# Kernel tuning notes

Hardware: AMD Instinct MI355X
Metric: run time of the kernel (lower is better)

## Reference

```python
import jax, jax.numpy as jnp
import numpy as np
import math

B, L, DM = 2, 2048, 1536
H, FD = 12, 16          # num_heads, feature_dim
DV = DM // H            # head_dim = 128
D2 = FD * FD            # expanded Taylor feature dim = 256
CHUNK = 128
EPS = 1e-12
LN_EPS = 1e-5


def setup_inputs() -> dict:
    key = jax.random.key(0)
    ks = jax.random.split(key, 5)
    s = lambda fan_in: 1.0 / math.sqrt(fan_in)
    return {
        "hidden_states": jax.random.normal(ks[0], (B, L, DM), jnp.float32),
        "Wq": jax.random.normal(ks[1], (DM, H * FD), jnp.float32) * s(DM),
        "Wk": jax.random.normal(ks[2], (DM, H * FD), jnp.float32) * s(DM),
        "Wv": jax.random.normal(ks[3], (DM, H * DV), jnp.float32) * s(DM),
        "Wo": jax.random.normal(ks[4], (H * DV, DM), jnp.float32) * s(H * DV),
        "ln_q_g": jnp.ones((H * FD,), jnp.float32),
        "ln_q_b": jnp.zeros((H * FD,), jnp.float32),
        "ln_k_g": jnp.ones((H * FD,), jnp.float32),
        "ln_k_b": jnp.zeros((H * FD,), jnp.float32),
    }


def _layernorm(x, g, b):
    mu = x.mean(-1, keepdims=True)
    var = ((x - mu) ** 2).mean(-1, keepdims=True)
    return (x - mu) * jax.lax.rsqrt(var + LN_EPS) * g + b


def _taylor_exp(x):
    # x: (b, h, l, d) -> flattened outer product / sqrt(d): (b, h, l, d*d)
    x2 = x[..., :, None] * x[..., None, :]
    return x2.reshape(*x.shape[:-1], -1) / math.sqrt(FD)


def _rebased_forward(hidden_states, Wq, Wk, Wv, Wo, ln_q_g, ln_q_b, ln_k_g, ln_k_b):
    b, l, _ = hidden_states.shape
    q = _layernorm(hidden_states @ Wq, ln_q_g, ln_q_b)
    k = _layernorm(hidden_states @ Wk, ln_k_g, ln_k_b)
    v = hidden_states @ Wv
    # (b, l, h*d) -> (b, h, l, d)
    q = q.reshape(b, l, H, FD).transpose(0, 2, 1, 3)
    k = k.reshape(b, l, H, FD).transpose(0, 2, 1, 3)
    v = v.reshape(b, l, H, DV).transpose(0, 2, 1, 3)
    q2 = _taylor_exp(q)  # (b, h, l, D2)
    k2 = _taylor_exp(k)

    nC = l // CHUNK
    # chunk-major layout for scan: (nC, b, h, C, .)
    q2c = q2.reshape(b, H, nC, CHUNK, D2).transpose(2, 0, 1, 3, 4)
    k2c = k2.reshape(b, H, nC, CHUNK, D2).transpose(2, 0, 1, 3, 4)
    vc = v.reshape(b, H, nC, CHUNK, DV).transpose(2, 0, 1, 3, 4)
    mask = jnp.tril(jnp.ones((CHUNK, CHUNK), q2.dtype))  # causal within chunk

    S0 = jnp.zeros((b, H, D2, DV), q2.dtype)  # running sum of k2^T v
    z0 = jnp.zeros((b, H, D2), q2.dtype)      # running sum of k2

    def step(carry, inp):
        S, z = carry
        qc, kc, vcur = inp
        A = jnp.einsum("bhcd,bhed->bhce", qc, kc) * mask  # intra-chunk scores
        num = jnp.einsum("bhcd,bhdv->bhcv", qc, S) + jnp.einsum("bhce,bhev->bhcv", A, vcur)
        den = jnp.einsum("bhcd,bhd->bhc", qc, z) + A.sum(-1)
        o = num / (den[..., None] + EPS)
        S = S + jnp.einsum("bhed,bhev->bhdv", kc, vcur)
        z = z + kc.sum(2)
        return (S, z), o

    _, o = jax.lax.scan(step, (S0, z0), (q2c, k2c, vc))
    # (nC, b, h, C, dv) -> (b, l, h*dv)
    o = o.transpose(1, 2, 0, 3, 4).reshape(b, H, l, DV).transpose(0, 2, 1, 3).reshape(b, l, H * DV)
    return o @ Wo


def reference(hidden_states, Wq, Wk, Wv, Wo, ln_q_g, ln_q_b, ln_k_g, ln_k_b):
    return _rebased_forward(hidden_states, Wq, Wk, Wv, Wo, ln_q_g, ln_q_b, ln_k_g, ln_k_b)
```

## Files before the change

### kernel.cpp

```cpp
#include <hip/hip_runtime.h>
#include <hip/hip_bf16.h>
#include <math.h>

#define Bc   2
#define Lc   2048
#define DMc  1536
#define Hc   12
#define FDc  16
#define DVc  128
#define D2c  256
#define CHK  128
#define NCH  16
#define ROWS (Bc*Lc)
#define HFD  (Hc*FDc)
#define HDV  (Hc*DVc)
#define NQK  (2*HFD)
#define NPRJ (NQK + HDV)

typedef __bf16 bf16x8 __attribute__((ext_vector_type(8)));
typedef float f32x4 __attribute__((ext_vector_type(4)));

__device__ __forceinline__ float bf2f(unsigned short u) {
    return __uint_as_float(((unsigned int)u) << 16);
}
__device__ __forceinline__ unsigned short f2bf(float v) {
    unsigned int u = __float_as_uint(v);
    unsigned int r = (u + 0x7FFFu + ((u >> 16) & 1u)) >> 16;
    return (unsigned short)r;
}
__device__ __forceinline__ unsigned int pack2(unsigned short a, unsigned short b) {
    return (unsigned int)a | ((unsigned int)b << 16);
}
__device__ __forceinline__ float ldin(const void* p, size_t i, int isf32) {
    return isf32 ? ((const float*)p)[i] : bf2f(((const unsigned short*)p)[i]);
}

#define GLL16(g, l) __builtin_amdgcn_global_load_lds( \
    (const __attribute__((address_space(1))) unsigned int*)(g), \
    (__attribute__((address_space(3))) unsigned int*)(l), 16, 0, 0)

__global__ void probe_dtype(const unsigned short* __restrict__ hs, int* __restrict__ flag) {
    const int tid = threadIdx.x;
    int sane = 0;
    for (int i = tid; i < 1024; i += 256) {
        unsigned short b = hs[2 * i];
        int e = (b >> 7) & 0xFF;
        if (e >= 97 && e <= 157) sane++;
    }
    __shared__ int tot;
    if (tid == 0) tot = 0;
    __syncthreads();
    atomicAdd(&tot, sane);
    __syncthreads();
    if (tid == 0) *flag = (tot >= 614) ? 0 : 1;
}

__global__ __launch_bounds__(256) void conv_bf16(const void* __restrict__ X,
                                                 unsigned short* __restrict__ Y,
                                                 int n4, const int* __restrict__ flagp) {
    const int f = *flagp;
    int i = blockIdx.x * 256 + threadIdx.x;
    if (i >= n4) return;
    if (f) {
        float4 x = ((const float4*)X)[i];
        ushort4 y;
        y.x = f2bf(x.x); y.y = f2bf(x.y); y.z = f2bf(x.z); y.w = f2bf(x.w);
        ((ushort4*)Y)[i] = y;
    } else {
        ((ushort4*)Y)[i] = ((const ushort4*)X)[i];
    }
}

__global__ __launch_bounds__(256) void convT_all(const void* __restrict__ Wq,
                                                 const void* __restrict__ Wk,
                                                 const void* __restrict__ Wv,
                                                 const void* __restrict__ Wo,
                                                 unsigned short* __restrict__ Wqkvt,
                                                 unsigned short* __restrict__ Wot,
                                                 const int* __restrict__ flagp) {
    const int f = *flagp;
    __shared__ float tile[64][65];
    const int t = threadIdx.x;
    int id = blockIdx.x;
    const void* W; unsigned short* Wt; int rows, cols, bx, by;
    if (id < 72)       { W = Wq; Wt = Wqkvt;                          rows = DMc; cols = HFD; bx = (id % 3) * 64;  by = (id / 3) * 64; }
    else if (id < 144) { id -= 72;  W = Wk; Wt = Wqkvt + (size_t)HFD * DMc; rows = DMc; cols = HFD; bx = (id % 3) * 64;  by = (id / 3) * 64; }
    else if (id < 720) { id -= 144; W = Wv; Wt = Wqkvt + (size_t)NQK * DMc; rows = DMc; cols = HDV; bx = (id % 24) * 64; by = (id / 24) * 64; }
    else               { id -= 720; W = Wo; Wt = Wot;                 rows = HDV; cols = DMc; bx = (id % 24) * 64; by = (id / 24) * 64; }
#pragma unroll
    for (int u = 0; u < 16; u++) {
        int idx = t + u * 256;
        int r = idx >> 6, c = idx & 63;
        tile[r][c] = ldin(W, (size_t)(by + r) * cols + bx + c, f);
    }
    __syncthreads();
#pragma unroll
    for (int u = 0; u < 16; u++) {
        int idx = t + u * 256;
        int r = idx >> 6, c = idx & 63;
        Wt[(size_t)(bx + r) * rows + by + c] = f2bf(tile[c][r]);
    }
}

__global__ __launch_bounds__(512) void gemm_mfma_bt(const unsigned short* __restrict__ A,
                                                    const unsigned short* __restrict__ Bt,
                                                    void* __restrict__ C,
                                                    int M, int N, int K,
                                                    int ldc,
                                                    int cMode, const int* __restrict__ flagp,
                                                    unsigned short* __restrict__ vTout) {
    const int f = *flagp;
    __shared__ __align__(16) unsigned char smem[32768];
    unsigned short* As = (unsigned short*)smem;
    unsigned short* Bsu = As + 8192;
    f32x4* scr4 = (f32x4*)smem;

    const int tid = threadIdx.x;
    const int wave = tid >> 6, lane = tid & 63;
    const int kgrp = wave >> 2;
    const int w4 = wave & 3;
    const int lin = blockIdx.y * gridDim.x + blockIdx.x;
    const int nwg = gridDim.x * gridDim.y;
    const int swz = (lin & 7) * (nwg >> 3) + (lin >> 3);
    const int row0 = (swz / gridDim.x) * 128, col0 = (swz % gridDim.x) * 128;
    const int wrow = (w4 >> 1) * 64, wcol = (w4 & 1) * 64;
    const int mlane = lane & 15, quad = lane >> 4;
    const int kHalf = K >> 1;

    const unsigned short* Ab = A + (size_t)row0 * K + (size_t)kgrp * kHalf;
    const unsigned short* Bb = Bt + (size_t)col0 * K + (size_t)kgrp * kHalf;
    const int t256 = tid & 255;
    const int r0 = t256 >> 2;
    const int kc = (t256 & 3) * 8;
    const size_t off0 = (size_t)r0 * K + kc;
    const size_t off1 = (size_t)(r0 + 64) * K + kc;
    char* AsW = (char*)As + kgrp * 8192 + w4 * 1024;
    char* BsW = (char*)Bsu + kgrp * 8192 + w4 * 1024;
    const int ldsBase = kgrp * 4096;

    f32x4 acc[4][4] = {};

    for (int k0 = 0; k0 < kHalf; k0 += 32) {
        GLL16(Ab + off0 + k0, AsW);
        GLL16(Ab + off1 + k0, AsW + 4096);
        GLL16(Bb + off0 + k0, BsW);
        GLL16(Bb + off1 + k0, BsW + 4096);
        __syncthreads();
        bf16x8 a[4], b[4];
#pragma unroll
        for (int i = 0; i < 4; i++)
            a[i] = *(const bf16x8*)&As[ldsBase + (wrow + i * 16 + mlane) * 32 + quad * 8];
#pragma unroll
        for (int j = 0; j < 4; j++)
            b[j] = *(const bf16x8*)&Bsu[ldsBase + (wcol + j * 16 + mlane) * 32 + quad * 8];
#pragma unroll
        for (int i = 0; i < 4; i++)
#pragma unroll
            for (int j = 0; j < 4; j++)
                acc[i][j] = __builtin_amdgcn_mfma_f32_16x16x32_bf16(a[i], b[j], acc[i][j], 0, 0, 0);
        __syncthreads();
    }

    {
        const int col = (wave & 1) * 64 + lane;
        if (kgrp == 1 && w4 < 2) {
#pragma unroll
            for (int i = 0; i < 4; i++)
#pragma unroll
                for (int j = 0; j < 4; j++)
                    scr4[(i * 4 + j) * 128 + col] = acc[i][j];
        }
        __syncthreads();
        if (kgrp == 0 && w4 < 2) {
#pragma unroll
            for (int i = 0; i < 4; i++)
#pragma unroll
                for (int j = 0; j < 4; j++)
                    acc[i][j] += scr4[(i * 4 + j) * 128 + col];
        }
        __syncthreads();
        if (kgrp == 1 && w4 >= 2) {
#pragma unroll
            for (int i = 0; i < 4; i++)
#pragma unroll
                for (int j = 0; j < 4; j++)
                    scr4[(i * 4 + j) * 128 + col] = acc[i][j];
        }
        __syncthreads();
        if (kgrp == 0 && w4 >= 2) {
#pragma unroll
            for (int i = 0; i < 4; i++)
#pragma unroll
                for (int j = 0; j < 4; j++)
                    acc[i][j] += scr4[(i * 4 + j) * 128 + col];
        }
    }
    if (kgrp != 0) return;

    float* Cf = nullptr;
    unsigned short* Cb16 = nullptr;
    bool doT = false;
    int tOff = 0;
    if (cMode == 0) Cf = (float*)C;
    else if (cMode == 1) Cb16 = (unsigned short*)C;
    else if (cMode == 2) { if (f) Cf = (float*)C; else Cb16 = (unsigned short*)C; }
    else if (cMode == 4) {
        if (col0 < NQK) Cf = (float*)C;
        else { doT = true; tOff = NQK; }
    }
    if (cMode <= 3 && vTout) doT = true;

#pragma unroll
    for (int i = 0; i < 4; i++)
#pragma unroll
        for (int j = 0; j < 4; j++) {
            const int col = col0 + wcol + j * 16 + mlane;
            if (Cf) {
#pragma unroll
                for (int r = 0; r < 4; r++) {
                    const int row = row0 + wrow + i * 16 + quad * 4 + r;
                    Cf[(size_t)row * ldc + col] = acc[i][j][r];
                }
            } else if (Cb16) {
#pragma unroll
                for (int r = 0; r < 4; r++) {
                    const int row = row0 + wrow + i * 16 + quad * 4 + r;
                    Cb16[(size_t)row * ldc + col] = f2bf(acc[i][j][r]);
                }
            }
            if (doT) {
                ushort4 pk;
                pk.x = f2bf(acc[i][j][0]); pk.y = f2bf(acc[i][j][1]);
                pk.z = f2bf(acc[i][j][2]); pk.w = f2bf(acc[i][j][3]);
                *(ushort4*)(vTout + (size_t)(col - tOff) * M + row0 + wrow + i * 16 + quad * 4) = pk;
            }
        }
}

__global__ __launch_bounds__(192) void ln_kernel(const float* __restrict__ qk,
                                                 float* __restrict__ q, float* __restrict__ k,
                                                 const void* __restrict__ gq,
                                                 const void* __restrict__ bq,
                                                 const void* __restrict__ gk,
                                                 const void* __restrict__ bk,
                                                 const int* __restrict__ flagp) {
    const int f = *flagp;
    const int row = blockIdx.x, t = threadIdx.x;
    float vq = qk[(size_t)row * NQK + t];
    float vk = qk[(size_t)row * NQK + HFD + t];
    float s[4] = {vq, vq * vq, vk, vk * vk};
    __shared__ float part[4][3];
    const int w = t >> 6, lane = t & 63;
#pragma unroll
    for (int i = 0; i < 4; i++) {
        float v = s[i];
        for (int off = 32; off; off >>= 1) v += __shfl_down(v, off);
        if (lane == 0) part[i][w] = v;
    }
    __syncthreads();
    float sq  = part[0][0] + part[0][1] + part[0][2];
    float sq2 = part[1][0] + part[1][1] + part[1][2];
    float sk  = part[2][0] + part[2][1] + part[2][2];
    float sk2 = part[3][0] + part[3][1] + part[3][2];
    const float inv = 1.0f / (float)HFD;
    float muq = sq * inv, muk = sk * inv;
    float varq = sq2 * inv - muq * muq;
    float vark = sk2 * inv - muk * muk;
    float oq = (vq - muq) * rsqrtf(varq + 1e-5f) * ldin(gq, t, f) + ldin(bq, t, f);
    float ok = (vk - muk) * rsqrtf(vark + 1e-5f) * ldin(gk, t, f) + ldin(bk, t, f);
    q[(size_t)row * HFD + t] = oq;
    k[(size_t)row * HFD + t] = ok;
}

__global__ __launch_bounds__(256) void state_prefix_mfma(const float* __restrict__ kn,
                                                         const unsigned short* __restrict__ vT,
                                                         unsigned short* __restrict__ St,
                                                         float* __restrict__ zc) {
    const int bx = blockIdx.x;
    const int by = blockIdx.y;
    const int bh = blockIdx.z;
    const int h = bh % Hc, b = bh / Hc;
    const int t0 = bx * 16;
    const int tid = threadIdx.x;
    const int wave = tid >> 6, lane = tid & 63;
    const int mlane = lane & 15, quad = lane >> 4;

    __shared__ __align__(16) float kcs[CHK * FDc];
    __shared__ __align__(16) unsigned short K2t[16 * 136];
    __shared__ __align__(16) unsigned short Vs[64 * 136];
    __shared__ float zp[16][17];
    __shared__ float zpre[16];
    if (tid < 16) zpre[tid] = 0.f;

    f32x4 acc = {};
    const int kr = tid >> 1, khf = tid & 1;
    const int d2l = tid & 15, cg = tid >> 4;
    const int vrow = tid >> 2, vseg = tid & 3;
    const int dvL = wave * 16 + mlane;

    for (int n = 0; n < NCH; n++) {
        const int row0 = b * Lc + n * CHK;
        __syncthreads();
        {
            const float4* src = (const float4*)(kn + (size_t)(row0 + kr) * HFD + h * FDc + khf * 8);
            *(float4*)(kcs + kr * 16 + khf * 8)     = src[0];
            *(float4*)(kcs + kr * 16 + khf * 8 + 4) = src[1];
            const uint4* g = (const uint4*)(vT + (size_t)(h * 128 + by * 64 + vrow) * ROWS + row0 + vseg * 32);
            *(uint4*)(Vs + vrow * 136 + vseg * 32)      = g[0];
            *(uint4*)(Vs + vrow * 136 + vseg * 32 + 8)  = g[1];
            *(uint4*)(Vs + vrow * 136 + vseg * 32 + 16) = g[2];
            *(uint4*)(Vs + vrow * 136 + vseg * 32 + 24) = g[3];
        }
        __syncthreads();
        {
            float zs_ = 0.f;
            unsigned short pk[8];
#pragma unroll
            for (int u = 0; u < 8; u++) {
                int c = cg * 8 + u;
                float p = kcs[c * 16 + bx] * kcs[c * 16 + d2l] * 0.25f;
                zs_ += p;
                pk[u] = f2bf(p);
            }
            uint4 w;
            w.x = pack2(pk[0], pk[1]); w.y = pack2(pk[2], pk[3]);
            w.z = pack2(pk[4], pk[5]); w.w = pack2(pk[6], pk[7]);
            *(uint4*)(K2t + d2l * 136 + cg * 8) = w;
            zp[d2l][cg] = zs_;
        }
        __syncthreads();
        {
            size_t base = (((size_t)(bh * NCH + n) * 16 + bx) * 128) * 16;
            int dv = by * 64 + dvL;
            ushort4 pk;
            pk.x = f2bf(acc[0]); pk.y = f2bf(acc[1]);
            pk.z = f2bf(acc[2]); pk.w = f2bf(acc[3]);
            *(ushort4*)(St + base + (size_t)dv * 16 + quad * 4) = pk;
            if (tid < 16) {
                float s = 0.f;
#pragma unroll
                for (int c = 0; c < 16; c++) s += zp[tid][c];
                if (by == 0)
                    zc[(size_t)(bh * NCH + n) * D2c + t0 + tid] = zpre[tid];
                zpre[tid] += s;
            }
        }
        {
#pragma unroll
            for (int ks = 0; ks < 4; ks++) {
                bf16x8 a = *(const bf16x8*)(K2t + mlane * 136 + ks * 32 + quad * 8);
                bf16x8 bfr = *(const bf16x8*)(Vs + dvL * 136 + ks * 32 + quad * 8);
                acc = __builtin_amdgcn_mfma_f32_16x16x32_bf16(a, bfr, acc, 0, 0, 0);
            }
        }
    }
}

__global__ __launch_bounds__(256) void chunk_out_mfma(const float* __restrict__ qn,
                                                      const float* __restrict__ kn,
                                                      const unsigned short* __restrict__ St,
                                                      const float* __restrict__ z,
                                                      const unsigned short* __restrict__ vT,
                                                      unsigned short* __restrict__ o) {
    const int blk = blockIdx.x;
    const int n = blk & 15, bh = blk >> 4;
    const int h = bh % Hc, b = bh / Hc;
    const int row0 = b * Lc + n * CHK;
    const int tid = threadIdx.x;
    const int wave = tid >> 6, lane = tid & 63;
    const int mlane = lane & 15, quad = lane >> 4;
    const int wrow = (wave >> 1) * 64, wcol = (wave & 1) * 64;

    __shared__ __align__(16) unsigned char lds[61952];
    float* Qs   = (float*)lds;
    float* zs   = (float*)(lds + 8192);
    float* denp = (float*)(lds + 9216);
    float* dinv = (float*)(lds + 10240);
    unsigned char* U = lds + 10752;
    unsigned short* Q2s = (unsigned short*)U;
    unsigned short* Sts = (unsigned short*)(U + 10240);
    unsigned short* Kb  = (unsigned short*)U;
    unsigned short* Qb  = (unsigned short*)(U + 8192);
    unsigned short* At  = (unsigned short*)(U + 16384);
    unsigned short* Vs  = (unsigned short*)U;

    {
        int r = tid >> 1, hf = tid & 1;
        const float4* src = (const float4*)(qn + (size_t)(row0 + r) * HFD + h * FDc + hf * 8);
        *(float4*)(Qs + r * 16 + hf * 8)     = src[0];
        *(float4*)(Qs + r * 16 + hf * 8 + 4) = src[1];
        if (tid < 64)
            ((float4*)zs)[tid] = ((const float4*)(z + ((size_t)bh * NCH + n) * D2c))[tid];
    }
    __syncthreads();

    const int qc = tid >> 1, qhalf = tid & 1;
    float qr[16];
#pragma unroll
    for (int ff = 0; ff < 16; ff++) qr[ff] = Qs[qc * 16 + ff];

    f32x4 acc[4][4] = {};
    float den1 = 0.f;
    const unsigned short* Stb = St + ((size_t)bh * NCH + n) * ((size_t)D2c * DVc);

    for (int k0 = 0; k0 < 256; k0 += 32) {
        {
            unsigned short pk[16];
#pragma unroll
            for (int kk = 0; kk < 16; kk++) {
                int d2 = k0 + qhalf * 16 + kk;
                float val = qr[d2 >> 4] * qr[d2 & 15] * 0.25f;
                den1 += val * zs[d2];
                pk[kk] = f2bf(val);
            }
            uint4 w0, w1;
            w0.x = pack2(pk[0], pk[1]);  w0.y = pack2(pk[2], pk[3]);
            w0.z = pack2(pk[4], pk[5]);  w0.w = pack2(pk[6], pk[7]);
            w1.x = pack2(pk[8], pk[9]);  w1.y = pack2(pk[10], pk[11]);
            w1.z = pack2(pk[12], pk[13]); w1.w = pack2(pk[14], pk[15]);
            *(uint4*)(Q2s + qc * 40 + qhalf * 16) = w0;
            *(uint4*)(Q2s + qc * 40 + qhalf * 16 + 8) = w1;
        }
        {
            int r = tid >> 1, hf = tid & 1;
            const uint4* g = (const uint4*)(Stb + (size_t)((k0 >> 4) + hf) * 2048 + r * 16);
            uint4 d0 = g[0], d1 = g[1];
            *(uint4*)(Sts + r * 40 + hf * 16) = d0;
            *(uint4*)(Sts + r * 40 + hf * 16 + 8) = d1;
        }
        __syncthreads();
        bf16x8 a[4], bfr[4];
#pragma unroll
        for (int i = 0; i < 4; i++)
            a[i] = *(const bf16x8*)(Q2s + (wrow + i * 16 + mlane) * 40 + quad * 8);
#pragma unroll
        for (int j = 0; j < 4; j++)
            bfr[j] = *(const bf16x8*)(Sts + (wcol + j * 16 + mlane) * 40 + quad * 8);
#pragma unroll
        for (int i = 0; i < 4; i++)
#pragma unroll
            for (int j = 0; j < 4; j++)
                acc[i][j] = __builtin_amdgcn_mfma_f32_16x16x32_bf16(a[i], bfr[j], acc[i][j], 0, 0, 0);
        __syncthreads();
    }
    denp[qhalf * 128 + qc] = den1;

    {
        int r = tid >> 1, hf = tid & 1;
        if (hf == 0) {
            unsigned short pq[16], pkk[16];
#pragma unroll
            for (int ff = 0; ff < 16; ff++) pq[ff] = f2bf(Qs[r * 16 + ff]);
            const float* kg = kn + (size_t)(row0 + r) * HFD + h * FDc;
#pragma unroll
            for (int ff = 0; ff < 16; ff++) pkk[ff] = f2bf(kg[ff]);
            uint4 w;
            w.x = pack2(pq[0], pq[1]);  w.y = pack2(pq[2], pq[3]);
            w.z = pack2(pq[4], pq[5]);  w.w = pack2(pq[6], pq[7]);
            *(uint4*)(Qb + r * 32) = w;
            w.x = pack2(pq[8], pq[9]);  w.y = pack2(pq[10], pq[11]);
            w.z = pack2(pq[12], pq[13]); w.w = pack2(pq[14], pq[15]);
            *(uint4*)(Qb + r * 32 + 8) = w;
            w.x = pack2(pkk[0], pkk[1]);  w.y = pack2(pkk[2], pkk[3]);
            w.z = pack2(pkk[4], pkk[5]);  w.w = pack2(pkk[6], pkk[7]);
            *(uint4*)(Kb + r * 32) = w;
            w.x = pack2(pkk[8], pkk[9]);  w.y = pack2(pkk[10], pkk[11]);
            w.z = pack2(pkk[12], pkk[13]); w.w = pack2(pkk[14], pkk[15]);
            *(uint4*)(Kb + r * 32 + 8) = w;
        } else {
            uint4 zz = make_uint4(0, 0, 0, 0);
            *(uint4*)(Qb + r * 32 + 16) = zz;
            *(uint4*)(Qb + r * 32 + 24) = zz;
            *(uint4*)(Kb + r * 32 + 16) = zz;
            *(uint4*)(Kb + r * 32 + 24) = zz;
        }
    }
    __syncthreads();

    {
        f32x4 pacc[4][4] = {};
        bf16x8 a[4], bfr[4];
#pragma unroll
        for (int i = 0; i < 4; i++)
            a[i] = *(const bf16x8*)(Qb + (wrow + i * 16 + mlane) * 32 + quad * 8);
#pragma unroll
        for (int j = 0; j < 4; j++)
            bfr[j] = *(const bf16x8*)(Kb + (wcol + j * 16 + mlane) * 32 + quad * 8);
#pragma unroll
        for (int i = 0; i < 4; i++)
#pragma unroll
            for (int j = 0; j < 4; j++)
                pacc[i][j] = __builtin_amdgcn_mfma_f32_16x16x32_bf16(a[i], bfr[j], pacc[i][j], 0, 0, 0);
#pragma unroll
        for (int i = 0; i < 4; i++)
#pragma unroll
            for (int j = 0; j < 4; j++) {
                int e = wcol + j * 16 + mlane;
#pragma unroll
                for (int r = 0; r < 4; r++) {
                    int c = wrow + i * 16 + quad * 4 + r;
                    float p = pacc[i][j][r];
                    float aval = (e <= c) ? p * p * 0.0625f : 0.f;
                    At[c * 136 + e] = f2bf(aval);
                }
            }
    }
    __syncthreads();

    if (tid < 128) {
        float rs = 0.f;
#pragma unroll
        for (int e8 = 0; e8 < 128; e8 += 8) {
            bf16x8 v8 = *(const bf16x8*)(At + tid * 136 + e8);
#pragma unroll
            for (int u = 0; u < 8; u++) rs += (float)v8[u];
        }
        dinv[tid] = 1.0f / (denp[tid] + denp[128 + tid] + rs + 1e-12f);
    }

    for (int e0 = 0; e0 < 128; e0 += 32) {
        {
            int r = tid >> 1, hf = tid & 1;
            const uint4* g = (const uint4*)(vT + (size_t)(h * 128 + r) * ROWS + row0 + e0 + hf * 16);
            uint4 d0 = g[0], d1 = g[1];
            *(uint4*)(Vs + r * 40 + hf * 16) = d0;
            *(uint4*)(Vs + r * 40 + hf * 16 + 8) = d1;
        }
        __syncthreads();
        bf16x8 a[4], bfr[4];
#pragma unroll
        for (int i = 0; i < 4; i++)
            a[i] = *(const bf16x8*)(At + (wrow + i * 16 + mlane) * 136 + e0 + quad * 8);
#pragma unroll
        for (int j = 0; j < 4; j++)
            bfr[j] = *(const bf16x8*)(Vs + (wcol + j * 16 + mlane) * 40 + quad * 8);
#pragma unroll
        for (int i = 0; i < 4; i++)
#pragma unroll
            for (int j = 0; j < 4; j++)
                acc[i][j] = __builtin_amdgcn_mfma_f32_16x16x32_bf16(a[i], bfr[j], acc[i][j], 0, 0, 0);
        __syncthreads();
    }

#pragma unroll
    for (int i = 0; i < 4; i++)
#pragma unroll
        for (int j = 0; j < 4; j++) {
            int col = h * 128 + wcol + j * 16 + mlane;
#pragma unroll
            for (int r = 0; r < 4; r++) {
                int c = wrow + i * 16 + quad * 4 + r;
                o[(size_t)(row0 + c) * HDV + col] = f2bf(acc[i][j][r] * dinv[c]);
            }
        }
}

extern "C" void kernel_launch(void* const* d_in, const int* in_sizes, int n_in,
                              void* d_out, int out_size, void* d_ws, size_t ws_size,
                              hipStream_t stream) {
    const void* hs = d_in[0];
    const void* Wq = d_in[1];
    const void* Wk = d_in[2];
    const void* Wv = d_in[3];
    const void* Wo = d_in[4];
    const void* gq = d_in[5];
    const void* bq = d_in[6];
    const void* gk = d_in[7];
    const void* bk = d_in[8];

    int* flag = (int*)d_ws;
    float* base = (float*)d_ws + 16;
    float* qpre = base;
    float* kpre = qpre + (size_t)ROWS * HFD;
    float* vreg = kpre + (size_t)ROWS * HFD;
    float* Sc   = vreg + (size_t)ROWS * HDV;
    float* zc   = Sc + (size_t)Bc * Hc * NCH * D2c * DVc;
    float* fend = zc + (size_t)Bc * Hc * NCH * D2c;
    unsigned short* hsb = (unsigned short*)fend;
    unsigned short* ob  = hsb;
    unsigned short* Wot = hsb + (size_t)ROWS * DMc;
    unsigned short* vT  = Wot + (size_t)HDV * DMc;
    float* qk = Sc;
    unsigned short* Wqkvt = (unsigned short*)(Sc + (size_t)ROWS * NQK);
    unsigned short* St = (unsigned short*)vreg;

    probe_dtype<<<1, 256, 0, stream>>>((const unsigned short*)hs, flag);

    conv_bf16<<<(ROWS * DMc / 4 + 255) / 256, 256, 0, stream>>>(hs, hsb, ROWS * DMc / 4, flag);
    convT_all<<<1296, 256, 0, stream>>>(Wq, Wk, Wv, Wo, Wqkvt, Wot, flag);

    gemm_mfma_bt<<<dim3(NPRJ / 128, ROWS / 128), 512, 0, stream>>>(
        hsb, Wqkvt, qk, ROWS, NPRJ, DMc, NQK, 4, flag, vT);

    ln_kernel<<<ROWS, HFD, 0, stream>>>(qk, qpre, kpre, gq, bq, gk, bk, flag);

    state_prefix_mfma<<<dim3(16, 2, Bc * Hc), 256, 0, stream>>>(kpre, vT, St, zc);

    chunk_out_mfma<<<Bc * Hc * NCH, 256, 0, stream>>>(qpre, kpre, St, zc, vT, ob);

    gemm_mfma_bt<<<dim3(DMc / 128, ROWS / 128), 512, 0, stream>>>(
        ob, Wot, d_out, ROWS, DMc, HDV, DMc, 2, flag, nullptr);
}
```

Baseline: 242.5 us.

## Double-buffer LDS tiles in bf16 MFMA GEMM to overlap global loads

```diff
diff --git a/kernel.cpp b/kernel.cpp
--- a/kernel.cpp
+++ b/kernel.cpp
@@ -110,9 +110,8 @@
                                                     int cMode, const int* __restrict__ flagp,
                                                     unsigned short* __restrict__ vTout) {
     const int f = *flagp;
-    __shared__ __align__(16) unsigned char smem[32768];
-    unsigned short* As = (unsigned short*)smem;
-    unsigned short* Bsu = As + 8192;
+    __shared__ __align__(16) unsigned char smem[65536];
+    unsigned short* S16 = (unsigned short*)smem;
     f32x4* scr4 = (f32x4*)smem;
 
     const int tid = threadIdx.x;
@@ -134,32 +133,54 @@
     const int kc = (t256 & 3) * 8;
     const size_t off0 = (size_t)r0 * K + kc;
     const size_t off1 = (size_t)(r0 + 64) * K + kc;
-    char* AsW = (char*)As + kgrp * 8192 + w4 * 1024;
-    char* BsW = (char*)Bsu + kgrp * 8192 + w4 * 1024;
-    const int ldsBase = kgrp * 4096;
+    const int stA = kgrp * 8192 + w4 * 1024;
 
     f32x4 acc[4][4] = {};
-
-    for (int k0 = 0; k0 < kHalf; k0 += 32) {
-        GLL16(Ab + off0 + k0, AsW);
-        GLL16(Ab + off1 + k0, AsW + 4096);
-        GLL16(Bb + off0 + k0, BsW);
-        GLL16(Bb + off1 + k0, BsW + 4096);
-        __syncthreads();
+    const int nt = kHalf >> 5;
+
+    {
+        char* dst = (char*)smem + stA;
+        GLL16(Ab + off0, dst);
+        GLL16(Ab + off1, dst + 4096);
+        GLL16(Bb + off0, dst + 16384);
+        GLL16(Bb + off1, dst + 16384 + 4096);
+    }
+
+    int cur = 0;
+    for (int t = 0; t < nt; ++t) {
+        if (t + 1 < nt) {
+            const int k0n = (t + 1) << 5;
+            char* dst = (char*)smem + (cur ^ 1) * 32768 + stA;
+            GLL16(Ab + off0 + k0n, dst);
+            GLL16(Ab + off1 + k0n, dst + 4096);
+            GLL16(Bb + off0 + k0n, dst + 16384);
+            GLL16(Bb + off1 + k0n, dst + 16384 + 4096);
+            asm volatile("s_waitcnt vmcnt(4)" ::: "memory");
+        } else {
+            asm volatile("s_waitcnt vmcnt(0)" ::: "memory");
+        }
+        __builtin_amdgcn_sched_barrier(0);
+        __builtin_amdgcn_s_barrier();
+        __builtin_amdgcn_sched_barrier(0);
+        const unsigned short* Ar = S16 + cur * 16384 + kgrp * 4096;
+        const unsigned short* Br = Ar + 8192;
         bf16x8 a[4], b[4];
 #pragma unroll
         for (int i = 0; i < 4; i++)
-            a[i] = *(const bf16x8*)&As[ldsBase + (wrow + i * 16 + mlane) * 32 + quad * 8];
+            a[i] = *(const bf16x8*)&Ar[(wrow + i * 16 + mlane) * 32 + quad * 8];
 #pragma unroll
         for (int j = 0; j < 4; j++)
-            b[j] = *(const bf16x8*)&Bsu[ldsBase + (wcol + j * 16 + mlane) * 32 + quad * 8];
+            b[j] = *(const bf16x8*)&Br[(wcol + j * 16 + mlane) * 32 + quad * 8];
 #pragma unroll
         for (int i = 0; i < 4; i++)
 #pragma unroll
             for (int j = 0; j < 4; j++)
                 acc[i][j] = __builtin_amdgcn_mfma_f32_16x16x32_bf16(a[i], b[j], acc[i][j], 0, 0, 0);
-        __syncthreads();
-    }
+        __builtin_amdgcn_sched_barrier(0);
+        __builtin_amdgcn_s_barrier();
+        cur ^= 1;
+    }
+    __syncthreads();
 
     {
         const int col = (wave & 1) * 64 + lane;
```

New measurement: 246.2 us. Within noise of the previous version (+1.5%).
